# Optimization experiments

Measured on AMD Instinct MI355X. Metric: run time of the kernel, lower is better.

Reference implementation:

```python
import jax, jax.numpy as jnp
import numpy as np

BSZ, L, H, P = 4, 4096, 1024, 512
DT_MIN, DT_MAX = 1e-3, 1e-1


def setup_inputs() -> dict:
    key = jax.random.key(0)
    ks = jax.random.split(key, 6)
    input_sequence = jax.random.normal(ks[0], (BSZ, 1, H, 1, L), jnp.float32)
    # hidden_state_method='zero': hiddens arg only has to carry the right shape
    hiddens = jnp.zeros((BSZ, 1, P), jnp.float32)
    # stable (left-half-plane) diagonal state matrix, like HiPPO-LegS eigenvalues
    Lambda_re = -0.5 * jax.random.uniform(ks[1], (P,), jnp.float32) - 0.1
    Lambda_im = jnp.pi * jnp.arange(P, dtype=jnp.float32)
    # B stored as (P, H, 2) real/imag pair (lecun-ish scale), C as (H, P, 2)
    B = jax.random.normal(ks[2], (P, H, 2), jnp.float32) / jnp.sqrt(2.0 * H)
    C = jax.random.normal(ks[3], (H, P, 2), jnp.float32) / jnp.sqrt(2.0 * P)
    D = jax.random.normal(ks[4], (H,), jnp.float32)
    log_step = jax.random.uniform(ks[5], (P, 1), jnp.float32,
                                  minval=float(np.log(DT_MIN)),
                                  maxval=float(np.log(DT_MAX)))
    return dict(input_sequence=input_sequence, hiddens=hiddens,
                Lambda_re=Lambda_re, Lambda_im=Lambda_im,
                B=B, C=C, D=D, log_step=log_step)


def _binop(qi, qj):
    # diagonal linear recurrence combine: x_j = A_j * x_i + b_j
    Ai, bi = qi
    Aj, bj = qj
    return (Aj * Ai, Aj * bi + bj)


def _s5_forward(input_sequence, Lambda_re, Lambda_im, B, C, D, log_step):
    Lam = jax.lax.complex(Lambda_re, Lambda_im)              # (P,)
    step = jnp.exp(log_step[:, 0])                           # (P,)
    # zero-order-hold discretization
    Lambda_bar = jnp.exp(Lam * step)                         # (P,) complex
    B_scale = (Lambda_bar - 1.0) / Lam                       # (P,) complex
    B_bar_re = B_scale.real[:, None] * B[..., 0] - B_scale.imag[:, None] * B[..., 1]
    B_bar_im = B_scale.real[:, None] * B[..., 1] + B_scale.imag[:, None] * B[..., 0]

    u = input_sequence[:, 0, :, 0].transpose(0, 2, 1)        # (BSZ, L, H) float32

    # Bu_t = B_bar @ u_t, done on real/imag parts to keep u real in the GEMM
    Bu = jax.lax.complex(jnp.einsum('blh,ph->blp', u, B_bar_re),
                         jnp.einsum('blh,ph->blp', u, B_bar_im))  # (BSZ,L,P)
    # prepend zero hidden state (hidden_state_method='zero')
    zeros0 = jnp.zeros((Bu.shape[0], 1, Bu.shape[2]), Bu.dtype)
    Bu_elems = jnp.concatenate([zeros0, Bu], axis=1)          # (BSZ,L+1,P)
    Lam_elems = jnp.broadcast_to(Lambda_bar, Bu_elems.shape)  # (BSZ,L+1,P)

    _, xs = jax.lax.associative_scan(_binop, (Lam_elems, Bu_elems), axis=1)
    xs = xs[:, 1:]                                            # (BSZ,L,P) complex states

    # conj_sym=True: y_t = 2 * Re(C_tilde @ x_t)
    Cr, Ci = C[..., 0], C[..., 1]                             # (H,P) each
    ys = 2.0 * (jnp.einsum('hp,blp->blh', Cr, xs.real)
                - jnp.einsum('hp,blp->blh', Ci, xs.imag))     # (BSZ,L,H)
    ys = ys + D * u                                           # feedthrough
    ys = jax.nn.gelu(ys, approximate=False)                   # activation='gelu'
    return ys.transpose(0, 2, 1)[:, None, :, None, :]         # (BSZ,1,H,1,L)


def reference(input_sequence, hiddens, Lambda_re, Lambda_im, B, C, D, log_step):
    del hiddens  # unused with hidden_state_method='zero'
    return _s5_forward(input_sequence, Lambda_re, Lambda_im, B, C, D, log_step)
```

## Files before the change

### kernel.cpp

```cpp
#include <hip/hip_runtime.h>
#include <math.h>


constexpr int kB = 4, kL = 4096, kH = 1024, kP = 512;
constexpr int kM = 1024, kK = 1024, kN = 4096;

typedef short bf16x8 __attribute__((ext_vector_type(8)));
typedef float f32x4 __attribute__((ext_vector_type(4)));

constexpr size_t A1H_OFF = 0;
constexpr size_t A2H_OFF = A1H_OFF + (size_t)kM * kK * 2;
constexpr size_t LBAR_B  = A2H_OFF + (size_t)kM * kK * 2;
constexpr size_t BU_B    = (LBAR_B + 4096 + 255) & ~(size_t)255;
constexpr size_t TH_B    = BU_B + (size_t)kB * kM * kN * 4;
constexpr size_t MID_BYTES = TH_B + (size_t)kB * kN * kK * 2;

__device__ __forceinline__ unsigned short f2bf(float x) {
  unsigned int u = __float_as_uint(x);
  u += 0x7fffu + ((u >> 16) & 1u);
  return (unsigned short)(u >> 16);
}
__device__ __forceinline__ float bf2f(unsigned short h) {
  return __uint_as_float(((unsigned int)h) << 16);
}

__device__ __forceinline__ void gl2lds16(const void* g, void* l) {
  __builtin_amdgcn_global_load_lds(
      (const __attribute__((address_space(1))) void*)g,
      (__attribute__((address_space(3))) void*)l, 16, 0, 0);
}

template <int N>
__device__ __forceinline__ void wait_vm() {
  __builtin_amdgcn_s_waitcnt((N & 15) | ((N >> 4) << 14) | (15 << 8) | (7 << 4));
}

__global__ __launch_bounds__(256) void k_prep_tr(
    const float* __restrict__ Lre, const float* __restrict__ Lim,
    const float* __restrict__ B, const float* __restrict__ log_step,
    const float* __restrict__ C, unsigned char* __restrict__ ws,
    const float* __restrict__ in, unsigned short* __restrict__ oh) {
  int bid = blockIdx.x;
  if (bid < 4096) {
    __shared__ float t[64][65];
    int b = bid >> 10;
    int r0 = ((bid >> 6) & 15) * 64;
    int c0 = (bid & 63) * 64;
    int tid = threadIdx.x;
    const float* src = in + ((size_t)b * 1024 + r0) * 4096 + c0;
    int cc = (tid & 15) * 4, rr = tid >> 4;
#pragma unroll
    for (int i = 0; i < 4; i++) {
      float4 v = *(const float4*)(src + (size_t)(rr + i * 16) * 4096 + cc);
      t[rr + i * 16][cc + 0] = v.x;
      t[rr + i * 16][cc + 1] = v.y;
      t[rr + i * 16][cc + 2] = v.z;
      t[rr + i * 16][cc + 3] = v.w;
    }
    __syncthreads();
    int oc = tid >> 2;
    int og = (tid & 3) * 2;
#pragma unroll
    for (int i = 0; i < 2; i++) {
      int g = og + i;
      unsigned short hv[8];
#pragma unroll
      for (int j = 0; j < 8; j++) hv[j] = f2bf(t[g * 8 + j][oc]);
      size_t ob = ((size_t)b * 4096 + c0 + oc) * 1024 + r0 + g * 8;
      *(uint4*)(oh + ob) = *(uint4*)hv;
    }
  } else if (bid < 4096 + kP) {
    int p = bid - 4096;
    float lr = Lre[p], li = Lim[p];
    float step = expf(log_step[p]);
    float er = expf(lr * step);
    float sb, cb;
    sincosf(li * step, &sb, &cb);
    float lbr = er * cb, lbi = er * sb;
    float nr = lbr - 1.0f, ni = lbi;
    float inv = 1.0f / (lr * lr + li * li);
    float sr = (nr * lr + ni * li) * inv;
    float si = (ni * lr - nr * li) * inv;

    if (threadIdx.x == 0) ((float2*)(ws + LBAR_B))[p] = make_float2(lbr, lbi);

    unsigned short* a1h = (unsigned short*)(ws + A1H_OFF);
    const float* Brow = B + (size_t)p * kH * 2;
    for (int h = threadIdx.x; h < kH; h += 256) {
      float br = Brow[2 * h], bi = Brow[2 * h + 1];
      a1h[(size_t)p * kK + h] = f2bf(sr * br - si * bi);
      a1h[(size_t)(kP + p) * kK + h] = f2bf(sr * bi + si * br);
    }
  } else {
    int h = bid - 4096 - kP;
    unsigned short* a2h = (unsigned short*)(ws + A2H_OFF);
    for (int k = threadIdx.x; k < kK; k += 256) {
      float v = (k < kP) ? 2.f * C[((size_t)h * kP + k) * 2]
                         : -2.f * C[((size_t)h * kP + (k - kP)) * 2 + 1];
      a2h[(size_t)h * kK + k] = f2bf(v);
    }
  }
}

__global__ __launch_bounds__(256) void k_transpose_h(
    const unsigned short* __restrict__ in, unsigned short* __restrict__ oh) {
  __shared__ float t[64][65];
  int b = blockIdx.z;
  int r0 = blockIdx.y * 64;
  int c0 = blockIdx.x * 64;
  int tid = threadIdx.x;
  const unsigned short* src = in + ((size_t)b * 1024 + r0) * 4096 + c0;
  int cc = (tid & 7) * 8, rr = tid >> 3;
#pragma unroll
  for (int i = 0; i < 2; i++) {
    bf16x8 v = *(const bf16x8*)(src + (size_t)(rr + i * 32) * 4096 + cc);
#pragma unroll
    for (int j = 0; j < 8; j++)
      t[rr + i * 32][cc + j] = bf2f((unsigned short)v[j]);
  }
  __syncthreads();
  int oc = tid >> 2;
  int og = (tid & 3) * 2;
#pragma unroll
  for (int i = 0; i < 2; i++) {
    int g = og + i;
    unsigned short hv[8];
#pragma unroll
    for (int j = 0; j < 8; j++) hv[j] = f2bf(t[g * 8 + j][oc]);
    size_t ob = ((size_t)b * 4096 + c0 + oc) * 1024 + r0 + g * 8;
    *(uint4*)(oh + ob) = *(uint4*)hv;
  }
}


__device__ __forceinline__ int stage_src_off32(int Dp) {
  int Ds = Dp ^ (((Dp >> 9) & 1) << 5);
  int s = Ds >> 10, d = Ds & 1023;
  int row = (s << 4) + (d >> 6);
  int kk = (d & 63) >> 1;
  return row * kK + kk;
}

#define BAR __builtin_amdgcn_s_barrier()
#define LGKM0                                           \
  do {                                                  \
    asm volatile("s_waitcnt lgkmcnt(0)" ::: "memory");  \
    __builtin_amdgcn_sched_barrier(0);                  \
  } while (0)

template <bool EPI>
__global__ __launch_bounds__(512, 4) void k_gemm2p(
    const unsigned short* __restrict__ Ah, const unsigned short* __restrict__ Bh,
    void* __restrict__ outv, const float* __restrict__ u,
    const float* __restrict__ D) {
  __shared__ __align__(16) unsigned char lds[49152];
  constexpr int BUF = 24576;
  constexpr int NKT = kK / 32;

  int b = blockIdx.z;
  int m0 = blockIdx.y * 128, n0 = blockIdx.x * 256;
  int tid = threadIdx.x, w = tid >> 6;
  int q = (tid >> 4) & 3, r = tid & 15;
  int wm = (w >> 2) * 64, wn = (w & 3) * 64;
  int wmrb = (w >> 2) * 4, wnrb = (w & 3) * 4;
  int lane_off = (r * 64 + q * 16) ^ ((r & 8) << 2);

  int d0 = tid << 4;
  int rowk = stage_src_off32(d0);

  const unsigned short* pA = Ah + (size_t)m0 * kK;
  const unsigned short* pB = Bh + (size_t)b * kN * kK + (size_t)n0 * kK;

  f32x4 acc[4][4] = {};

#define STG(KT, LB)                                                       \
  do {                                                                    \
    gl2lds16(pA + (KT) * 32 + rowk, lds + (LB) + d0);                     \
    gl2lds16(pB + (KT) * 32 + rowk, lds + (LB) + 8192 + d0);              \
    gl2lds16(pB + (size_t)128 * kK + (KT) * 32 + rowk,                    \
             lds + (LB) + 16384 + d0);                                    \
  } while (0)

#define COMPUTE(LB)                                                       \
  do {                                                                    \
    bf16x8 a[4], bb[4];                                                   \
    _Pragma("unroll")                                                     \
    for (int mi = 0; mi < 4; mi++)                                        \
      a[mi] = *(const bf16x8*)(lds + (LB) + ((wmrb + mi) << 10) + lane_off); \
    _Pragma("unroll")                                                     \
    for (int nj = 0; nj < 4; nj++)                                        \
      bb[nj] = *(const bf16x8*)(lds + (LB) + 8192 +                       \
                                ((wnrb + nj) << 10) + lane_off);          \
    LGKM0;                                                                \
    __builtin_amdgcn_s_setprio(1);                                        \
    _Pragma("unroll")                                                     \
    for (int mi = 0; mi < 4; mi++)                                        \
      _Pragma("unroll")                                                   \
      for (int nj = 0; nj < 4; nj++)                                      \
        acc[mi][nj] = __builtin_amdgcn_mfma_f32_16x16x32_bf16(            \
            a[mi], bb[nj], acc[mi][nj], 0, 0, 0);                         \
    __builtin_amdgcn_s_setprio(0);                                        \
  } while (0)

  STG(0, 0);
  wait_vm<0>();
  BAR;

  for (int it = 0; it < NKT / 2; ++it) {
    int kt = it * 2;
    if (kt + 1 < NKT) STG(kt + 1, BUF);
    COMPUTE(0);
    wait_vm<0>();
    BAR;
    if (kt + 2 < NKT) STG(kt + 2, 0);
    COMPUTE(BUF);
    wait_vm<0>();
    BAR;
  }
#undef STG
#undef COMPUTE

  float* outf = (float*)outv;
  unsigned short* outh = (unsigned short*)outv;
#pragma unroll
  for (int mi = 0; mi < 4; mi++) {
#pragma unroll
    for (int reg = 0; reg < 4; reg++) {
      int row = m0 + wm + mi * 16 + q * 4 + reg;
      float dv = EPI ? D[row] : 0.f;
#pragma unroll
      for (int ni = 0; ni < 4; ni++) {
        int col = n0 + wn + ni * 16 + r;
        size_t o = ((size_t)b * kM + row) * (size_t)kN + col;
        float v = acc[mi][ni][reg];
        if (EPI) {
          float y = v + dv * u[o];
          outf[o] = 0.5f * y * (1.f + erff(y * 0.70710678118654752f));
        } else {
          outh[o] = f2bf(v);
        }
      }
    }
  }
}

__global__ __launch_bounds__(256) void k_scan(
    const unsigned short* __restrict__ buh, const float2* __restrict__ lbar,
    unsigned short* __restrict__ xsh) {
  int p = blockIdx.x & (kP - 1);
  int b = blockIdx.x >> 9;
  int tid = threadIdx.x, lane = tid & 63, w = tid >> 6;
  float2 lam = lbar[p];
  const unsigned short* sre = buh + ((size_t)b * kM + p) * (size_t)kN;
  const unsigned short* sim = sre + (size_t)kP * kN;

  float vr[16], vi[16];
  {
    const bf16x8* pr = (const bf16x8*)(sre + tid * 16);
    const bf16x8* pi = (const bf16x8*)(sim + tid * 16);
#pragma unroll
    for (int i = 0; i < 2; i++) {
      bf16x8 a = pr[i], c = pi[i];
#pragma unroll
      for (int j = 0; j < 8; j++) {
        vr[8 * i + j] = bf2f((unsigned short)a[j]);
        vi[8 * i + j] = bf2f((unsigned short)c[j]);
      }
    }
  }

  float xr = 0.f, xi = 0.f;
#pragma unroll
  for (int i = 0; i < 16; i++) {
    float nr2 = fmaf(lam.x, xr, fmaf(-lam.y, xi, vr[i]));
    float ni2 = fmaf(lam.x, xi, fmaf(lam.y, xr, vi[i]));
    xr = nr2; xi = ni2;
  }

  float Ar = lam.x, Ai = lam.y;
#pragma unroll
  for (int s = 0; s < 4; s++) {
    float tr = Ar * Ar - Ai * Ai, ti = 2.f * Ar * Ai;
    Ar = tr; Ai = ti;
  }
  float br = xr, bi = xi;

  for (int off = 1; off < 64; off <<= 1) {
    float pAr = __shfl_up(Ar, off), pAi = __shfl_up(Ai, off);
    float pbr = __shfl_up(br, off), pbi = __shfl_up(bi, off);
    if (lane >= off) {
      float nAr = Ar * pAr - Ai * pAi;
      float nAi = Ar * pAi + Ai * pAr;
      float nbr = Ar * pbr - Ai * pbi + br;
      float nbi = Ar * pbi + Ai * pbr + bi;
      Ar = nAr; Ai = nAi; br = nbr; bi = nbi;
    }
  }

  __shared__ float4 wtot[4];
  if (lane == 63) wtot[w] = make_float4(Ar, Ai, br, bi);
  __syncthreads();

  float eAr = __shfl_up(Ar, 1), eAi = __shfl_up(Ai, 1);
  float ebr = __shfl_up(br, 1), ebi = __shfl_up(bi, 1);
  if (lane == 0) { eAr = 1.f; eAi = 0.f; ebr = 0.f; ebi = 0.f; }

  float pAr = 1.f, pAi = 0.f, pbr = 0.f, pbi = 0.f;
  for (int j = 0; j < w; j++) {
    float4 t = wtot[j];
    float nAr = t.x * pAr - t.y * pAi;
    float nAi = t.x * pAi + t.y * pAr;
    float nbr = t.x * pbr - t.y * pbi + t.z;
    float nbi = t.x * pbi + t.y * pbr + t.w;
    pAr = nAr; pAi = nAi; pbr = nbr; pbi = nbi;
  }

  float initr = eAr * pbr - eAi * pbi + ebr;
  float initi = eAr * pbi + eAi * pbr + ebi;

  xr = initr; xi = initi;
  __align__(16) unsigned short hr[16], him[16];
#pragma unroll
  for (int i = 0; i < 16; i++) {
    float nr2 = fmaf(lam.x, xr, fmaf(-lam.y, xi, vr[i]));
    float ni2 = fmaf(lam.x, xi, fmaf(lam.y, xr, vi[i]));
    xr = nr2; xi = ni2;
    hr[i] = f2bf(nr2); him[i] = f2bf(ni2);
  }
  unsigned short* drh = xsh + ((size_t)b * kM + p) * (size_t)kN + tid * 16;
  unsigned short* dih = drh + (size_t)kP * kN;
  ((uint4*)drh)[0] = *(uint4*)&hr[0];
  ((uint4*)drh)[1] = *(uint4*)&hr[8];
  ((uint4*)dih)[0] = *(uint4*)&him[0];
  ((uint4*)dih)[1] = *(uint4*)&him[8];
}

constexpr size_t OBBAR = 0;
constexpr size_t OLBAR = (size_t)kP * kH;
constexpr size_t OBU = OLBAR + 1024;

__global__ __launch_bounds__(256) void k_precomputeF(
    const float* __restrict__ Lre, const float* __restrict__ Lim,
    const float* __restrict__ B, const float* __restrict__ log_step,
    float2* __restrict__ ws) {
  int p = blockIdx.x;
  float lr = Lre[p], li = Lim[p];
  float step = expf(log_step[p]);
  float er = expf(lr * step);
  float sb, cb;
  sincosf(li * step, &sb, &cb);
  float lbr = er * cb, lbi = er * sb;
  float nr = lbr - 1.0f, ni = lbi;
  float inv = 1.0f / (lr * lr + li * li);
  float sr = (nr * lr + ni * li) * inv;
  float si = (ni * lr - nr * li) * inv;
  if (threadIdx.x == 0) ws[OLBAR + p] = make_float2(lbr, lbi);
  float2* Bbar = ws + OBBAR;
  const float* Brow = B + (size_t)p * kH * 2;
  for (int h = threadIdx.x; h < kH; h += 256) {
    float br = Brow[2 * h], bi = Brow[2 * h + 1];
    Bbar[(size_t)p * kH + h] = make_float2(sr * br - si * bi, sr * bi + si * br);
  }
}

__global__ __launch_bounds__(256) void k_gemm1F(
    const float2* __restrict__ ws_bbar, const float* __restrict__ u,
    float2* __restrict__ Bu) {
  __shared__ float2 As[16][64];
  __shared__ float Bs[16][64];
  int b = blockIdx.z, m0 = blockIdx.y * 64, n0 = blockIdx.x * 64;
  int tid = threadIdx.x, tn = tid & 15, tm = tid >> 4;
  const float* uB = u + (size_t)b * kH * kL;
  float2 acc[4][4];
#pragma unroll
  for (int i = 0; i < 4; i++)
#pragma unroll
    for (int j = 0; j < 4; j++) acc[i][j] = make_float2(0.f, 0.f);
  int ar = tid >> 2, ac = (tid & 3) * 4, bk = tid >> 4, bc = (tid & 15) * 4;
  for (int k0 = 0; k0 < kH; k0 += 16) {
    const float4* src = (const float4*)(ws_bbar + (size_t)(m0 + ar) * kH + k0 + ac);
    float4 v01 = src[0], v23 = src[1];
    As[ac + 0][ar] = make_float2(v01.x, v01.y);
    As[ac + 1][ar] = make_float2(v01.z, v01.w);
    As[ac + 2][ar] = make_float2(v23.x, v23.y);
    As[ac + 3][ar] = make_float2(v23.z, v23.w);
    float4 v = *(const float4*)(uB + (size_t)(k0 + bk) * kL + n0 + bc);
    *(float4*)&Bs[bk][bc] = v;
    __syncthreads();
#pragma unroll
    for (int kk = 0; kk < 16; ++kk) {
      const float4* arow = (const float4*)&As[kk][0];
      float4 a01 = arow[tm * 2 + 0], a23 = arow[tm * 2 + 1];
      float2 a[4] = {make_float2(a01.x, a01.y), make_float2(a01.z, a01.w),
                     make_float2(a23.x, a23.y), make_float2(a23.z, a23.w)};
      float4 bv = ((const float4*)&Bs[kk][0])[tn];
      float bbv[4] = {bv.x, bv.y, bv.z, bv.w};
#pragma unroll
      for (int mi = 0; mi < 4; mi++)
#pragma unroll
        for (int ni = 0; ni < 4; ni++) {
          acc[mi][ni].x = fmaf(a[mi].x, bbv[ni], acc[mi][ni].x);
          acc[mi][ni].y = fmaf(a[mi].y, bbv[ni], acc[mi][ni].y);
        }
    }
    __syncthreads();
  }
  float2* BuB = Bu + (size_t)b * kP * kL;
#pragma unroll
  for (int mi = 0; mi < 4; mi++) {
    int row = m0 + tm * 4 + mi;
    float2* dst = BuB + (size_t)row * kL + n0 + tn * 4;
    ((float4*)dst)[0] = make_float4(acc[mi][0].x, acc[mi][0].y, acc[mi][1].x, acc[mi][1].y);
    ((float4*)dst)[1] = make_float4(acc[mi][2].x, acc[mi][2].y, acc[mi][3].x, acc[mi][3].y);
  }
}

__global__ __launch_bounds__(256) void k_scanF(float2* __restrict__ Bu,
                                               const float2* __restrict__ Lbar) {
  int p = blockIdx.x & (kP - 1);
  int b = blockIdx.x >> 9;
  int tid = threadIdx.x, lane = tid & 63, w = tid >> 6;
  float2 lam = Lbar[p];
  float2* seq = Bu + ((size_t)b * kP + p) * kL;
  float2 v[16];
  const float4* src = (const float4*)(seq + tid * 16);
#pragma unroll
  for (int i = 0; i < 8; i++) {
    float4 t = src[i];
    v[2 * i] = make_float2(t.x, t.y);
    v[2 * i + 1] = make_float2(t.z, t.w);
  }
  float xr = 0.f, xi = 0.f;
#pragma unroll
  for (int i = 0; i < 16; i++) {
    float nr2 = fmaf(lam.x, xr, fmaf(-lam.y, xi, v[i].x));
    float ni2 = fmaf(lam.x, xi, fmaf(lam.y, xr, v[i].y));
    xr = nr2; xi = ni2;
  }
  float Ar = lam.x, Ai = lam.y;
#pragma unroll
  for (int s = 0; s < 4; s++) {
    float tr = Ar * Ar - Ai * Ai, ti = 2.f * Ar * Ai;
    Ar = tr; Ai = ti;
  }
  float br = xr, bi = xi;
  for (int off = 1; off < 64; off <<= 1) {
    float pAr = __shfl_up(Ar, off), pAi = __shfl_up(Ai, off);
    float pbr = __shfl_up(br, off), pbi = __shfl_up(bi, off);
    if (lane >= off) {
      float nAr = Ar * pAr - Ai * pAi, nAi = Ar * pAi + Ai * pAr;
      float nbr = Ar * pbr - Ai * pbi + br, nbi = Ar * pbi + Ai * pbr + bi;
      Ar = nAr; Ai = nAi; br = nbr; bi = nbi;
    }
  }
  __shared__ float4 wtot[4];
  if (lane == 63) wtot[w] = make_float4(Ar, Ai, br, bi);
  __syncthreads();
  float eAr = __shfl_up(Ar, 1), eAi = __shfl_up(Ai, 1);
  float ebr = __shfl_up(br, 1), ebi = __shfl_up(bi, 1);
  if (lane == 0) { eAr = 1.f; eAi = 0.f; ebr = 0.f; ebi = 0.f; }
  float pAr = 1.f, pAi = 0.f, pbr = 0.f, pbi = 0.f;
  for (int j = 0; j < w; j++) {
    float4 t = wtot[j];
    float nAr = t.x * pAr - t.y * pAi, nAi = t.x * pAi + t.y * pAr;
    float nbr = t.x * pbr - t.y * pbi + t.z, nbi = t.x * pbi + t.y * pbr + t.w;
    pAr = nAr; pAi = nAi; pbr = nbr; pbi = nbi;
  }
  float initr = eAr * pbr - eAi * pbi + ebr;
  float initi = eAr * pbi + eAi * pbr + ebi;
  xr = initr; xi = initi;
  float4* dst = (float4*)(seq + tid * 16);
#pragma unroll
  for (int i = 0; i < 8; i++) {
    float nr0 = fmaf(lam.x, xr, fmaf(-lam.y, xi, v[2 * i].x));
    float ni0 = fmaf(lam.x, xi, fmaf(lam.y, xr, v[2 * i].y));
    float nr1 = fmaf(lam.x, nr0, fmaf(-lam.y, ni0, v[2 * i + 1].x));
    float ni1 = fmaf(lam.x, ni0, fmaf(lam.y, nr0, v[2 * i + 1].y));
    dst[i] = make_float4(nr0, ni0, nr1, ni1);
    xr = nr1; xi = ni1;
  }
}

__global__ __launch_bounds__(256) void k_gemm2F(
    const float2* __restrict__ C, const float2* __restrict__ X,
    const float* __restrict__ u, const float* __restrict__ D,
    float* __restrict__ out) {
  __shared__ float2 As[16][64];
  __shared__ float2 Bs[16][64];
  int b = blockIdx.z, m0 = blockIdx.y * 64, n0 = blockIdx.x * 64;
  int tid = threadIdx.x, tn = tid & 15, tm = tid >> 4;
  const float2* Xb = X + (size_t)b * kP * kL;
  float acc[4][4];
#pragma unroll
  for (int i = 0; i < 4; i++)
#pragma unroll
    for (int j = 0; j < 4; j++) acc[i][j] = 0.f;
  int ar = tid >> 2, ac = (tid & 3) * 4, bk = tid >> 4, bc = (tid & 15) * 4;
  for (int k0 = 0; k0 < kP; k0 += 16) {
    const float4* src = (const float4*)(C + (size_t)(m0 + ar) * kP + k0 + ac);
    float4 v01 = src[0], v23 = src[1];
    As[ac + 0][ar] = make_float2(v01.x, v01.y);
    As[ac + 1][ar] = make_float2(v01.z, v01.w);
    As[ac + 2][ar] = make_float2(v23.x, v23.y);
    As[ac + 3][ar] = make_float2(v23.z, v23.w);
    const float4* srcb = (const float4*)(Xb + (size_t)(k0 + bk) * kL + n0 + bc);
    ((float4*)&Bs[bk][bc])[0] = srcb[0];
    ((float4*)&Bs[bk][bc])[1] = srcb[1];
    __syncthreads();
#pragma unroll
    for (int kk = 0; kk < 16; ++kk) {
      const float4* arow = (const float4*)&As[kk][0];
      float4 a01 = arow[tm * 2 + 0], a23 = arow[tm * 2 + 1];
      float2 a[4] = {make_float2(a01.x, a01.y), make_float2(a01.z, a01.w),
                     make_float2(a23.x, a23.y), make_float2(a23.z, a23.w)};
      const float4* brow = (const float4*)&Bs[kk][0];
      float4 b01 = brow[tn * 2 + 0], b23 = brow[tn * 2 + 1];
      float2 bbv[4] = {make_float2(b01.x, b01.y), make_float2(b01.z, b01.w),
                       make_float2(b23.x, b23.y), make_float2(b23.z, b23.w)};
#pragma unroll
      for (int mi = 0; mi < 4; mi++)
#pragma unroll
        for (int ni = 0; ni < 4; ni++) {
          acc[mi][ni] = fmaf(a[mi].x, bbv[ni].x, acc[mi][ni]);
          acc[mi][ni] = fmaf(-a[mi].y, bbv[ni].y, acc[mi][ni]);
        }
    }
    __syncthreads();
  }
#pragma unroll
  for (int mi = 0; mi < 4; mi++) {
    int h = m0 + tm * 4 + mi;
    float d = D[h];
    const float* urow = u + ((size_t)b * kH + h) * kL + n0 + tn * 4;
    float4 uv = *(const float4*)urow;
    float uu[4] = {uv.x, uv.y, uv.z, uv.w};
    float res[4];
#pragma unroll
    for (int ni = 0; ni < 4; ni++) {
      float y = 2.f * acc[mi][ni] + d * uu[ni];
      res[ni] = 0.5f * y * (1.f + erff(y * 0.70710678118654752f));
    }
    float* orow = out + ((size_t)b * kH + h) * kL + n0 + tn * 4;
    *(float4*)orow = make_float4(res[0], res[1], res[2], res[3]);
  }
}

extern "C" void kernel_launch(void* const* d_in, const int* in_sizes, int n_in,
                              void* d_out, int out_size, void* d_ws, size_t ws_size,
                              hipStream_t stream) {
  const float* input_sequence = (const float*)d_in[0];
  const float* Lambda_re = (const float*)d_in[2];
  const float* Lambda_im = (const float*)d_in[3];
  const float* B = (const float*)d_in[4];
  const float* C = (const float*)d_in[5];
  const float* D = (const float*)d_in[6];
  const float* log_step = (const float*)d_in[7];
  float* out = (float*)d_out;

  if (ws_size >= MID_BYTES) {
    unsigned char* ws = (unsigned char*)d_ws;
    unsigned short* a1h = (unsigned short*)(ws + A1H_OFF);
    unsigned short* a2h = (unsigned short*)(ws + A2H_OFF);
    float2* lbar = (float2*)(ws + LBAR_B);
    unsigned short* th = (unsigned short*)(ws + TH_B);
    unsigned short* buh = (unsigned short*)(ws + BU_B);
    unsigned short* xsh = th;
    unsigned short* xshT = (unsigned short*)(ws + BU_B);

    k_prep_tr<<<dim3(4096 + kP + kH), 256, 0, stream>>>(
        Lambda_re, Lambda_im, B, log_step, C, ws, input_sequence, th);

    dim3 tgrid(kL / 64, 1024 / 64, kB);
    dim3 ggrid(kN / 256, kM / 128, kB);

    k_gemm2p<false><<<ggrid, 512, 0, stream>>>(a1h, th, buh, nullptr, nullptr);
    k_scan<<<dim3(kB * kP), 256, 0, stream>>>(buh, lbar, xsh);
    k_transpose_h<<<tgrid, 256, 0, stream>>>(xsh, xshT);
    k_gemm2p<true><<<ggrid, 512, 0, stream>>>(a2h, xshT, out, input_sequence, D);
  } else {
    float2* ws = (float2*)d_ws;
    float2* Bbar = ws + OBBAR;
    float2* Lbar = ws + OLBAR;
    float2* Bu = ws + OBU;
    k_precomputeF<<<dim3(kP), 256, 0, stream>>>(Lambda_re, Lambda_im, B, log_step, ws);
    k_gemm1F<<<dim3(kL / 64, kP / 64, kB), 256, 0, stream>>>(Bbar, input_sequence, Bu);
    k_scanF<<<dim3(kB * kP), 256, 0, stream>>>(Bu, Lbar);
    k_gemm2F<<<dim3(kL / 64, kH / 64, kB), 256, 0, stream>>>(
        (const float2*)C, (const float2*)Bu, input_sequence, D, out);
  }
}
```

Measured before the change: 248.8 us.

## Fuse transpose of scan states into second GEMM via K-major B loads

Removes the separate bf16 transpose kernel between the scan and the output GEMM. A new GEMM kernel reads the scan output in its natural (P-major, L-contiguous) layout, staging it to LDS with a custom address map and gathering B fragments with scalar 16-bit LDS reads. This saves a full read and write of the state tensor and one launch. In exchange, B-fragment loads from LDS become many small reads, which may cost bandwidth or bank conflicts inside the GEMM inner loop.

```diff
diff --git a/kernel.cpp b/kernel.cpp
--- a/kernel.cpp
+++ b/kernel.cpp
@@ -99,36 +99,6 @@
                          : -2.f * C[((size_t)h * kP + (k - kP)) * 2 + 1];
       a2h[(size_t)h * kK + k] = f2bf(v);
     }
-  }
-}
-
-__global__ __launch_bounds__(256) void k_transpose_h(
-    const unsigned short* __restrict__ in, unsigned short* __restrict__ oh) {
-  __shared__ float t[64][65];
-  int b = blockIdx.z;
-  int r0 = blockIdx.y * 64;
-  int c0 = blockIdx.x * 64;
-  int tid = threadIdx.x;
-  const unsigned short* src = in + ((size_t)b * 1024 + r0) * 4096 + c0;
-  int cc = (tid & 7) * 8, rr = tid >> 3;
-#pragma unroll
-  for (int i = 0; i < 2; i++) {
-    bf16x8 v = *(const bf16x8*)(src + (size_t)(rr + i * 32) * 4096 + cc);
-#pragma unroll
-    for (int j = 0; j < 8; j++)
-      t[rr + i * 32][cc + j] = bf2f((unsigned short)v[j]);
-  }
-  __syncthreads();
-  int oc = tid >> 2;
-  int og = (tid & 3) * 2;
-#pragma unroll
-  for (int i = 0; i < 2; i++) {
-    int g = og + i;
-    unsigned short hv[8];
-#pragma unroll
-    for (int j = 0; j < 8; j++) hv[j] = f2bf(t[g * 8 + j][oc]);
-    size_t ob = ((size_t)b * 4096 + c0 + oc) * 1024 + r0 + g * 8;
-    *(uint4*)(oh + ob) = *(uint4*)hv;
   }
 }
 
@@ -239,6 +209,105 @@
         } else {
           outh[o] = f2bf(v);
         }
+      }
+    }
+  }
+}
+
+
+__device__ __forceinline__ int bwin_src(int wv) {
+  int lg = wv >> 10, rem = wv & 1023;
+  int im = (rem >> 7) & 7, qm = (rem >> 5) & 3, c = (rem >> 4) & 1;
+  return (qm * 8 + im) * kN + lg * 16 + c * 8;
+}
+
+__global__ __launch_bounds__(512, 4) void k_gemm2t(
+    const unsigned short* __restrict__ Ah, const unsigned short* __restrict__ Xs,
+    float* __restrict__ out, const float* __restrict__ u,
+    const float* __restrict__ D) {
+  __shared__ __align__(16) unsigned char lds[49152];
+  constexpr int BUF = 24576;
+  constexpr int NKT = kK / 32;
+
+  int b = blockIdx.z;
+  int m0 = blockIdx.y * 128, n0 = blockIdx.x * 256;
+  int tid = threadIdx.x, w = tid >> 6;
+  int q = (tid >> 4) & 3, r = tid & 15;
+  int wm = (w >> 2) * 64, wn = (w & 3) * 64;
+  int wmrb = (w >> 2) * 4;
+  int lane_off = (r * 64 + q * 16) ^ ((r & 8) << 2);
+
+  int d0 = tid << 4;
+  int rowk = stage_src_off32(d0);
+  int bo1 = bwin_src(d0);
+  int bo2 = bwin_src(8192 + d0);
+
+  const unsigned short* pA = Ah + (size_t)m0 * kK;
+  const unsigned short* pX = Xs + (size_t)b * ((size_t)kM * kN) + n0;
+
+  f32x4 acc[4][4] = {};
+
+#define STG2(KT, LB)                                                      \
+  do {                                                                    \
+    gl2lds16(pA + (KT) * 32 + rowk, lds + (LB) + d0);                     \
+    gl2lds16(pX + (size_t)(KT) * 32 * kN + bo1, lds + (LB) + 8192 + d0);  \
+    gl2lds16(pX + (size_t)(KT) * 32 * kN + bo2, lds + (LB) + 16384 + d0); \
+  } while (0)
+
+#define COMPUTE2(LB)                                                      \
+  do {                                                                    \
+    bf16x8 a[4], bb[4];                                                   \
+    _Pragma("unroll")                                                     \
+    for (int mi = 0; mi < 4; mi++)                                        \
+      a[mi] = *(const bf16x8*)(lds + (LB) + ((wmrb + mi) << 10) + lane_off); \
+    const unsigned char* bb_base =                                        \
+        lds + (LB) + 8192 + r * 2 + q * 32 + ((w & 3) * 4) * 1024;        \
+    _Pragma("unroll")                                                     \
+    for (int nj = 0; nj < 4; nj++)                                        \
+      _Pragma("unroll")                                                   \
+      for (int i = 0; i < 8; i++)                                         \
+        bb[nj][i] = *(const short*)(bb_base + nj * 1024 + i * 128);       \
+    LGKM0;                                                                \
+    __builtin_amdgcn_s_setprio(1);                                        \
+    _Pragma("unroll")                                                     \
+    for (int mi = 0; mi < 4; mi++)                                        \
+      _Pragma("unroll")                                                   \
+      for (int nj = 0; nj < 4; nj++)                                      \
+        acc[mi][nj] = __builtin_amdgcn_mfma_f32_16x16x32_bf16(            \
+            a[mi], bb[nj], acc[mi][nj], 0, 0, 0);                         \
+    __builtin_amdgcn_s_setprio(0);                                        \
+  } while (0)
+
+  STG2(0, 0);
+  wait_vm<0>();
+  BAR;
+
+  for (int it = 0; it < NKT / 2; ++it) {
+    int kt = it * 2;
+    if (kt + 1 < NKT) STG2(kt + 1, BUF);
+    COMPUTE2(0);
+    wait_vm<0>();
+    BAR;
+    if (kt + 2 < NKT) STG2(kt + 2, 0);
+    COMPUTE2(BUF);
+    wait_vm<0>();
+    BAR;
+  }
+#undef STG2
+#undef COMPUTE2
+
+#pragma unroll
+  for (int mi = 0; mi < 4; mi++) {
+#pragma unroll
+    for (int reg = 0; reg < 4; reg++) {
+      int row = m0 + wm + mi * 16 + q * 4 + reg;
+      float dv = D[row];
+#pragma unroll
+      for (int ni = 0; ni < 4; ni++) {
+        int col = n0 + wn + ni * 16 + r;
+        size_t o = ((size_t)b * kM + row) * (size_t)kN + col;
+        float y = acc[mi][ni][reg] + dv * u[o];
+        out[o] = 0.5f * y * (1.f + erff(y * 0.70710678118654752f));
       }
     }
   }
@@ -565,18 +634,15 @@
     unsigned short* th = (unsigned short*)(ws + TH_B);
     unsigned short* buh = (unsigned short*)(ws + BU_B);
     unsigned short* xsh = th;
-    unsigned short* xshT = (unsigned short*)(ws + BU_B);
 
     k_prep_tr<<<dim3(4096 + kP + kH), 256, 0, stream>>>(
         Lambda_re, Lambda_im, B, log_step, C, ws, input_sequence, th);
 
-    dim3 tgrid(kL / 64, 1024 / 64, kB);
     dim3 ggrid(kN / 256, kM / 128, kB);
 
     k_gemm2p<false><<<ggrid, 512, 0, stream>>>(a1h, th, buh, nullptr, nullptr);
     k_scan<<<dim3(kB * kP), 256, 0, stream>>>(buh, lbar, xsh);
-    k_transpose_h<<<tgrid, 256, 0, stream>>>(xsh, xshT);
-    k_gemm2p<true><<<ggrid, 512, 0, stream>>>(a2h, xshT, out, input_sequence, D);
+    k_gemm2t<<<ggrid, 512, 0, stream>>>(a2h, xsh, out, input_sequence, D);
   } else {
     float2* ws = (float2*)d_ws;
     float2* Bbar = ws + OBBAR;
```

New measurement: 245.6 us. Within noise of the previous version (-1.3%).
